# Kernel tuning notes

Hardware: AMD Instinct MI355X
Metric: run time of the kernel (lower is better)

## Reference

```python
import jax, jax.numpy as jnp
import numpy as np

N_NODES = 50000
N_EDGES = 800000
MUL = 32                      # multiplicity of 0e and 1o in node_feats
AVG_NUM_NEIGHBORS = 16.0
INV_SQRT3 = 1.0 / np.sqrt(3.0)


def setup_inputs() -> dict:
    key = jax.random.key(0)
    ks = jax.random.split(key, 7)
    return {
        "node_feats": jax.random.normal(ks[0], (N_NODES, 4 * MUL), dtype=jnp.float32),
        "edge_attrs": jax.random.normal(ks[1], (N_EDGES, 4), dtype=jnp.float32),
        "senders": jax.random.randint(ks[2], (N_EDGES,), 0, N_NODES, dtype=jnp.int64) if jax.config.jax_enable_x64 else jax.random.randint(ks[2], (N_EDGES,), 0, N_NODES, dtype=jnp.int32),
        "receivers": jax.random.randint(ks[3], (N_EDGES,), 0, N_NODES, dtype=jnp.int32),
        "w_mlp0": jax.random.normal(ks[4], (1, 64), dtype=jnp.float32),
        "w_mlp1": jax.random.normal(ks[5], (64, 64), dtype=jnp.float32),
        "w_mlp2": jax.random.normal(ks[6], (64, 4 * MUL), dtype=jnp.float32),
    }


def reference(node_feats, edge_attrs, senders, receivers, w_mlp0, w_mlp1, w_mlp2):
    # node_feats layout: [N, MUL] scalars (0e) then [N, MUL*3] flattened vectors (1o)
    s = node_feats[:, :MUL]                          # [N, MUL]   32x0e
    v = node_feats[:, MUL:].reshape(-1, MUL, 3)      # [N, MUL,3] 32x1o

    # gather sender features per edge
    s_e = s[senders]                                 # [E, MUL]
    v_e = v[senders]                                 # [E, MUL, 3]

    ea0 = edge_attrs[:, :1]                          # [E,1]  1x0e
    ea1 = edge_attrs[:, 1:4]                         # [E,3]  1x1o

    # equivariant tensor product with edge_attrs.filter(drop='0e') = 1x1o,
    # keeping only target irreps (0e,1o):
    #   0e x 1o -> 1o : scalar * vector
    tp_1o = s_e[:, :, None] * ea1[:, None, :]        # [E, MUL, 3]
    #   1o x 1o -> 0e : dot / sqrt(3)  (component normalization)
    tp_0e = jnp.einsum('eci,ei->ec', v_e, ea1) * INV_SQRT3  # [E, MUL]

    # concatenate([msgs.filter(target), tp]).regroup() -> 64x0e + 64x1o
    scalars = jnp.concatenate([s_e, tp_0e], axis=1)          # [E, 2*MUL]
    vectors = jnp.concatenate([v_e, tp_1o], axis=1)          # [E, 2*MUL, 3]

    # MLP gate on scalar edge attrs (e3nn MLP: no bias, 1/sqrt(fan_in), swish)
    h = jax.nn.swish(ea0 @ w_mlp0 / jnp.sqrt(1.0))           # [E,64]
    h = jax.nn.swish(h @ w_mlp1 / jnp.sqrt(64.0))            # [E,64]
    mix = h @ w_mlp2 / jnp.sqrt(64.0)                        # [E, 4*MUL]

    n_sc = 2 * MUL
    scalars = scalars * mix[:, :n_sc]                        # gate 0e
    vectors = vectors * mix[:, n_sc:, None]                  # gate 1o (one scalar per vector)

    msgs = jnp.concatenate([scalars, vectors.reshape(vectors.shape[0], -1)], axis=1)  # [E, 8*MUL]

    # scatter-add messages to receivers
    out = jax.ops.segment_sum(msgs, receivers, num_segments=N_NODES)  # [N, 8*MUL]
    return out / jnp.sqrt(AVG_NUM_NEIGHBORS)
```

## Files before the change

kernel.cpp:

```cpp
#include <hip/hip_runtime.h>
#include <hip/hip_fp16.h>
#include <cstdint>

#define N_NODES   50000
#define FEAT      128
#define OUTF      256
#define MAX_EDGES 800000
#define CAP       64
#define INV_SQRT3 0.57735026918962576f
#define NW        (64 + 64*64 + 64*128)
#define TB_BLKS   ((N_NODES * 32 + 255) / 256)

__device__ float    g_wf[NW];
__device__ uint16_t g_lut16[65536 * 128];
__device__ uint16_t g_tbl[N_NODES * FEAT];
__device__ int      g_flags[4];
__device__ int      g_cnt[N_NODES];
__device__ uint32_t g_slot[N_NODES * CAP];
__device__ unsigned char g_used[65536];

__device__ __forceinline__ float b2f(uint32_t b) {
    union { uint32_t u; float f; } v; v.u = b << 16; return v.f;
}
__device__ __forceinline__ uint32_t f2b_bits(float f) {
    union { float f; uint32_t u; } v; v.f = f;
    uint32_t u = v.u;
    u += 0x7fffu + ((u >> 16) & 1u);
    return u >> 16;
}
__device__ __forceinline__ float swishf(float x) {
    return x / (1.0f + __expf(-x));
}
__device__ __forceinline__ float sane(float x) {
    union { float f; uint32_t u; } v; v.f = x;
    return (((v.u >> 23) & 0xffu) >= 0x8Du) ? 0.0f : x;
}
__device__ __forceinline__ float loadf(const void* p, int i, int isbf) {
    return isbf ? b2f(((const uint16_t*)p)[i]) : ((const float*)p)[i];
}
__device__ __forceinline__ float h2f(uint32_t bits16) {
    return __half2float(__ushort_as_half((unsigned short)bits16));
}
__device__ __forceinline__ uint32_t f2h(float x) {
    return (uint32_t)__half_as_ushort(__float2half(x));
}

__global__ __launch_bounds__(256) void init_kernel(
    const void* nf, const void* ea, const void* w0, const void* w1, const void* w2,
    const int* snd, const int* rcv, int snd_force64, int n_edges)
{
    int bx = blockIdx.x, t = threadIdx.x;
    if (bx == 0) {
        __shared__ int viol[4];
        if (t < 4) viol[t] = 0;
        __syncthreads();
        {   int n = N_NODES * FEAT; int step = (n / 256) | 1;
            long long i = (long long)t * step;
            if (i < n) {
                uint32_t e = (((const uint16_t*)nf)[i] >> 7) & 0xffu;
                if (e > 140u) atomicOr(&viol[2], 1);
            } }
        {   int n = n_edges * 4; int step = (n / 256) | 1;
            long long i = (long long)t * step;
            if (i < n) {
                uint32_t e = (((const uint16_t*)ea)[i] >> 7) & 0xffu;
                if (e > 140u) atomicOr(&viol[3], 1);
            } }
        if (t < 64) {
            int i = 2 * t + 1;
            if (i < 2 * n_edges) {
                if (snd[i] != 0) atomicOr(&viol[0], 1);
                if (rcv[i] != 0) atomicOr(&viol[1], 1);
            }
        }
        __syncthreads();
        if (t == 0) {
            g_flags[0] = snd_force64 ? 1 : !viol[0];
            g_flags[1] = !viol[1];
            g_flags[2] = !viol[2];
            g_flags[3] = !viol[3];
        }
    } else if (bx <= 49) {
        __shared__ int wv[3];
        if (t < 3) wv[t] = 0;
        __syncthreads();
        if (t < 64) {
            uint32_t e = (((const uint16_t*)w0)[t] >> 7) & 0xffu;
            if (e > 140u) atomicOr(&wv[0], 1);
        }
        { int i = t * 17; if (i < 4096) {
            uint32_t e = (((const uint16_t*)w1)[i] >> 7) & 0xffu;
            if (e > 140u) atomicOr(&wv[1], 1); } }
        { int i = t * 33; if (i < 8192) {
            uint32_t e = (((const uint16_t*)w2)[i] >> 7) & 0xffu;
            if (e > 140u) atomicOr(&wv[2], 1); } }
        __syncthreads();
        int i = (bx - 1) * 256 + t;
        if (i < 64)             g_wf[i] = loadf(w0, i, !wv[0]);
        else if (i < 64 + 4096) g_wf[i] = loadf(w1, i - 64, !wv[1]);
        else if (i < NW)        g_wf[i] = loadf(w2, i - (64 + 4096), !wv[2]);
    } else if (bx <= 49 + TB_BLKS) {
        __shared__ int nv;
        if (t == 0) nv = 0;
        __syncthreads();
        {   int n = N_NODES * FEAT; int step = (n / 256) | 1;
            long long i = (long long)t * step;
            if (i < n) {
                uint32_t e = (((const uint16_t*)nf)[i] >> 7) & 0xffu;
                if (e > 140u) atomicOr(&nv, 1);
            } }
        __syncthreads();
        int f2l = !nv;
        int i = (bx - 50) * 256 + t;
        if (i < N_NODES * 32) {
            int node = i >> 5, c = i & 31;
            int rb = node * FEAT;
            float s  = loadf(nf, rb + c, f2l);
            float v0 = loadf(nf, rb + 32 + 3 * c + 0, f2l);
            float v1 = loadf(nf, rb + 32 + 3 * c + 1, f2l);
            float v2 = loadf(nf, rb + 32 + 3 * c + 2, f2l);
            uint32_t lo = f2h(s)  | (f2h(v0) << 16);
            uint32_t hi = f2h(v1) | (f2h(v2) << 16);
            ((uint2*)g_tbl)[i] = make_uint2(lo, hi);
        }
    } else {
        __shared__ int ev[2];
        if (t < 2) ev[t] = 0;
        __syncthreads();
        {   int n = n_edges * 4; int step = (n / 256) | 1;
            long long i = (long long)t * step;
            if (i < n) {
                uint32_t x = (((const uint16_t*)ea)[i] >> 7) & 0xffu;
                if (x > 140u) atomicOr(&ev[1], 1);
            } }
        if (t < 64) {
            int i = 2 * t + 1;
            if (i < 2 * n_edges) {
                if (rcv[i] != 0) atomicOr(&ev[0], 1);
            }
        }
        __syncthreads();
        int f1l = !ev[0];
        int f3l = !ev[1];
        int e = (bx - 50 - TB_BLKS) * 256 + t;
        if (e < n_edges) {
            int ri = f1l ? rcv[2 * e] : rcv[e];
            ri = min(max(ri, 0), N_NODES - 1);
            uint32_t b0 = f3l ? (uint32_t)((const uint16_t*)ea)[4 * e]
                              : f2b_bits(((const float*)ea)[4 * e]);
            g_used[b0 & 0xffffu] = 1;
            int p = atomicAdd(&g_cnt[ri], 1);
            if (p < CAP) __builtin_nontemporal_store((uint32_t)e, &g_slot[ri * CAP + p]);
        }
    }
}

__global__ __launch_bounds__(256) void lut_kernel() {
    __shared__ float sw[4096 + 8192];
    int w = blockIdx.x * 4 + (threadIdx.x >> 6);
    int lane = threadIdx.x & 63;
    for (int i = threadIdx.x; i < 4096 + 8192; i += 256)
        sw[i] = g_wf[64 + i];
    int f = (lane < 16) ? (g_used[w + lane * 4096] != 0) : 0;
    unsigned long long mask = __ballot(f) & 0xffffull;
    __syncthreads();
    if (!mask) return;
    const float* w1 = sw;
    const float* w2 = sw + 4096;
    float w0l = g_wf[lane];
    while (mask) {
        int k = __builtin_ctzll(mask);
        mask &= mask - 1;
        int r = w + k * 4096;
        float x = b2f((uint32_t)r);
        float h0 = swishf(x * w0l);
        float a = 0.f;
        #pragma unroll 8
        for (int kk = 0; kk < 64; ++kk)
            a += __shfl(h0, kk, 64) * w1[kk * 64 + lane];
        float h1 = swishf(a * 0.125f);
        float a0 = 0.f, a1 = 0.f;
        #pragma unroll 8
        for (int kk = 0; kk < 64; ++kk) {
            float h1k = __shfl(h1, kk, 64);
            a0 += h1k * w2[kk * 128 + lane];
            a1 += h1k * w2[kk * 128 + 64 + lane];
        }
        float s1c = 0.125f * 0.25f;
        float s0c = (lane >= 32) ? s1c * INV_SQRT3 : s1c;
        float pa = sane(a0 * s0c);
        float pb = sane(a1 * s1c);
        float qa = __shfl_xor(pa, 32, 64);
        float qb = __shfl_xor(pb, 32, 64);
        if (lane < 32) {
            uint32_t lo = f2h(pa) | (f2h(qa) << 16);
            uint32_t hi = f2h(pb) | (f2h(qb) << 16);
            ((uint2*)(g_lut16 + (size_t)r * 128))[lane] = make_uint2(lo, hi);
        }
    }
}

__global__ __launch_bounds__(256) void gather_kernel(
    const void* __restrict__ ea, const int* __restrict__ snd, void* __restrict__ out)
{
    int wid = (blockIdx.x * 256 + threadIdx.x) >> 6;
    int lane = threadIdx.x & 63;
    if (wid >= N_NODES) return;
    int c = lane & 31;
    int half = lane >> 5;
    const int f0 = g_flags[0], f2 = g_flags[2], f3 = g_flags[3];
    int deg = min(g_cnt[wid], CAP);
    if (lane == 0) g_cnt[wid] = 0;

    float o0 = 0.f, o1 = 0.f, o2 = 0.f, o3 = 0.f,
          o4 = 0.f, o5 = 0.f, o6 = 0.f, o7 = 0.f;

    uint32_t pk_p = 0;
    float ex_p = 0.f, ey_p = 0.f, ez_p = 0.f;
    if (lane < deg) {
        uint32_t e = __builtin_nontemporal_load(&g_slot[wid * CAP + lane]);
        uint32_t b0;
        if (f3) {
            uint2 w = ((const uint2*)ea)[e];
            b0 = w.x & 0xffffu;
            ex_p = b2f(w.x >> 16);
            ey_p = b2f(w.y & 0xffffu);
            ez_p = b2f(w.y >> 16);
        } else {
            float4 w = ((const float4*)ea)[e];
            b0 = f2b_bits(w.x) & 0xffffu;
            ex_p = w.y; ey_p = w.z; ez_p = w.w;
        }
        int s_ = f0 ? snd[2 * e] : snd[e];
        s_ = min(max(s_, 0), N_NODES - 1);
        pk_p = ((uint32_t)s_ << 16) | b0;
    }

    const uint2* tbl = (const uint2*)g_tbl;

    for (int j = 0; j < deg; j += 4) {
        int jjA = j + half, jjB = j + 2 + half;
        float gA = (jjA < deg) ? 1.0f : 0.0f;
        float gB = (jjB < deg) ? 1.0f : 0.0f;
        int jxA = (jjA < deg) ? jjA : 0;
        int jxB = (jjB < deg) ? jjB : 0;

        uint32_t pkA = (uint32_t)__shfl((int)pk_p, jxA, 64);
        uint32_t pkB = (uint32_t)__shfl((int)pk_p, jxB, 64);
        float exA = __shfl(ex_p, jxA, 64), eyA = __shfl(ey_p, jxA, 64), ezA = __shfl(ez_p, jxA, 64);
        float exB = __shfl(ex_p, jxB, 64), eyB = __shfl(ey_p, jxB, 64), ezB = __shfl(ez_p, jxB, 64);

        uint2 mAu = ((const uint2*)(g_lut16 + (size_t)(pkA & 0xffffu) * 128))[c];
        uint2 mBu = ((const uint2*)(g_lut16 + (size_t)(pkB & 0xffffu) * 128))[c];
        uint2 hA = tbl[(size_t)(pkA >> 16) * 32 + c];
        uint2 hB = tbl[(size_t)(pkB >> 16) * 32 + c];

        float sA  = h2f(hA.x & 0xffffu), vA0 = h2f(hA.x >> 16);
        float vA1 = h2f(hA.y & 0xffffu), vA2 = h2f(hA.y >> 16);
        float sB  = h2f(hB.x & 0xffffu), vB0 = h2f(hB.x >> 16);
        float vB1 = h2f(hB.y & 0xffffu), vB2 = h2f(hB.y >> 16);

        {
            float m0 = h2f(mAu.x & 0xffffu) * gA, m1 = h2f(mAu.x >> 16) * gA;
            float m2 = h2f(mAu.y & 0xffffu) * gA, m3 = h2f(mAu.y >> 16) * gA;
            o0 += sA * m0;
            o1 += (vA0 * exA + vA1 * eyA + vA2 * ezA) * m1;
            o2 += vA0 * m2; o3 += vA1 * m2; o4 += vA2 * m2;
            float sm3 = sA * m3;
            o5 += exA * sm3; o6 += eyA * sm3; o7 += ezA * sm3;
        }
        {
            float m0 = h2f(mBu.x & 0xffffu) * gB, m1 = h2f(mBu.x >> 16) * gB;
            float m2 = h2f(mBu.y & 0xffffu) * gB, m3 = h2f(mBu.y >> 16) * gB;
            o0 += sB * m0;
            o1 += (vB0 * exB + vB1 * eyB + vB2 * ezB) * m1;
            o2 += vB0 * m2; o3 += vB1 * m2; o4 += vB2 * m2;
            float sm3 = sB * m3;
            o5 += exB * sm3; o6 += eyB * sm3; o7 += ezB * sm3;
        }
    }

    o0 += __shfl_xor(o0, 32, 64);
    o1 += __shfl_xor(o1, 32, 64);
    o2 += __shfl_xor(o2, 32, 64);
    o3 += __shfl_xor(o3, 32, 64);
    o4 += __shfl_xor(o4, 32, 64);
    o5 += __shfl_xor(o5, 32, 64);
    o6 += __shfl_xor(o6, 32, 64);
    o7 += __shfl_xor(o7, 32, 64);

    if (half == 0) {
        size_t bo = (size_t)wid * OUTF;
        if (f2) {
            uint16_t* o = (uint16_t*)out;
            o[bo + c]             = (uint16_t)f2b_bits(o0);
            o[bo + 32 + c]        = (uint16_t)f2b_bits(o1);
            o[bo + 64 + 3*c + 0]  = (uint16_t)f2b_bits(o2);
            o[bo + 64 + 3*c + 1]  = (uint16_t)f2b_bits(o3);
            o[bo + 64 + 3*c + 2]  = (uint16_t)f2b_bits(o4);
            o[bo + 160 + 3*c + 0] = (uint16_t)f2b_bits(o5);
            o[bo + 160 + 3*c + 1] = (uint16_t)f2b_bits(o6);
            o[bo + 160 + 3*c + 2] = (uint16_t)f2b_bits(o7);
        } else {
            float* o = (float*)out;
            o[bo + c]             = o0;
            o[bo + 32 + c]        = o1;
            o[bo + 64 + 3*c + 0]  = o2;
            o[bo + 64 + 3*c + 1]  = o3;
            o[bo + 64 + 3*c + 2]  = o4;
            o[bo + 160 + 3*c + 0] = o5;
            o[bo + 160 + 3*c + 1] = o6;
            o[bo + 160 + 3*c + 2] = o7;
        }
    }
}

extern "C" void kernel_launch(void* const* d_in, const int* in_sizes, int n_in,
                              void* d_out, int out_size, void* d_ws, size_t ws_size,
                              hipStream_t stream) {
    (void)n_in; (void)out_size; (void)d_ws; (void)ws_size;
    const void* nf = d_in[0];
    const void* ea = d_in[1];
    const int* snd = (const int*)d_in[2];
    const int* rcv = (const int*)d_in[3];
    const void* w0 = d_in[4];
    const void* w1 = d_in[5];
    const void* w2 = d_in[6];

    int n_edges = in_sizes[1] / 4;
    if (n_edges > MAX_EDGES) n_edges = MAX_EDGES;
    int snd_force64 = (in_sizes[2] == 2 * in_sizes[3]) ? 1 : 0;
    int eb = (n_edges + 255) / 256;

    init_kernel<<<50 + TB_BLKS + eb, 256, 0, stream>>>(nf, ea, w0, w1, w2, snd, rcv, snd_force64, n_edges);
    lut_kernel<<<1024, 256, 0, stream>>>();
    gather_kernel<<<(N_NODES + 3) / 4, 256, 0, stream>>>(ea, snd, d_out);
}
```

Baseline: 243.8 us.

## Bin edges by receiver block then build per-node slots in shared memory

Replaces per-node global atomics into scattered slot arrays with a two-level bucketing: edges are first appended to 782 coarse bins (64 nodes each), then a second pass builds per-node slot lists in LDS and writes them out contiguously. The bin pass is fused into the LUT kernel launch as extra blocks, and the LUT blocks now read weights from global memory instead of staging them in shared memory. This aims to cut scattered global atomics and write traffic, at the cost of an extra read/write of edge indices and fixed bin capacity that may drop edges if a bin overflows.

```diff
diff --git a/kernel.cpp b/kernel.cpp
--- a/kernel.cpp
+++ b/kernel.cpp
@@ -10,13 +10,20 @@
 #define INV_SQRT3 0.57735026918962576f
 #define NW        (64 + 64*64 + 64*128)
 #define TB_BLKS   ((N_NODES * 32 + 255) / 256)
+#define NBINS     782
+#define BINCAP    1536
+#define NPAD      (NBINS * 64)
+
+typedef unsigned int u32x4 __attribute__((ext_vector_type(4)));
 
 __device__ float    g_wf[NW];
 __device__ uint16_t g_lut16[65536 * 128];
 __device__ uint16_t g_tbl[N_NODES * FEAT];
 __device__ int      g_flags[4];
-__device__ int      g_cnt[N_NODES];
-__device__ uint32_t g_slot[N_NODES * CAP];
+__device__ int      g_cnt[NPAD];
+__device__ uint32_t g_slot[NPAD * CAP];
+__device__ uint32_t g_bin[NBINS * BINCAP];
+__device__ int      g_bcnt[NBINS];
 __device__ unsigned char g_used[65536];
 
 __device__ __forceinline__ float b2f(uint32_t b) {
@@ -149,54 +156,75 @@
             uint32_t b0 = f3l ? (uint32_t)((const uint16_t*)ea)[4 * e]
                               : f2b_bits(((const float*)ea)[4 * e]);
             g_used[b0 & 0xffffu] = 1;
-            int p = atomicAdd(&g_cnt[ri], 1);
-            if (p < CAP) __builtin_nontemporal_store((uint32_t)e, &g_slot[ri * CAP + p]);
-        }
-    }
-}
-
-__global__ __launch_bounds__(256) void lut_kernel() {
-    __shared__ float sw[4096 + 8192];
-    int w = blockIdx.x * 4 + (threadIdx.x >> 6);
-    int lane = threadIdx.x & 63;
-    for (int i = threadIdx.x; i < 4096 + 8192; i += 256)
-        sw[i] = g_wf[64 + i];
-    int f = (lane < 16) ? (g_used[w + lane * 4096] != 0) : 0;
-    unsigned long long mask = __ballot(f) & 0xffffull;
-    __syncthreads();
-    if (!mask) return;
-    const float* w1 = sw;
-    const float* w2 = sw + 4096;
-    float w0l = g_wf[lane];
-    while (mask) {
-        int k = __builtin_ctzll(mask);
-        mask &= mask - 1;
-        int r = w + k * 4096;
-        float x = b2f((uint32_t)r);
-        float h0 = swishf(x * w0l);
-        float a = 0.f;
-        #pragma unroll 8
-        for (int kk = 0; kk < 64; ++kk)
-            a += __shfl(h0, kk, 64) * w1[kk * 64 + lane];
-        float h1 = swishf(a * 0.125f);
-        float a0 = 0.f, a1 = 0.f;
-        #pragma unroll 8
-        for (int kk = 0; kk < 64; ++kk) {
-            float h1k = __shfl(h1, kk, 64);
-            a0 += h1k * w2[kk * 128 + lane];
-            a1 += h1k * w2[kk * 128 + 64 + lane];
-        }
-        float s1c = 0.125f * 0.25f;
-        float s0c = (lane >= 32) ? s1c * INV_SQRT3 : s1c;
-        float pa = sane(a0 * s0c);
-        float pb = sane(a1 * s1c);
-        float qa = __shfl_xor(pa, 32, 64);
-        float qb = __shfl_xor(pb, 32, 64);
-        if (lane < 32) {
-            uint32_t lo = f2h(pa) | (f2h(qa) << 16);
-            uint32_t hi = f2h(pb) | (f2h(qb) << 16);
-            ((uint2*)(g_lut16 + (size_t)r * 128))[lane] = make_uint2(lo, hi);
-        }
+            int bin = ri >> 6;
+            int p = atomicAdd(&g_bcnt[bin], 1);
+            if (p < BINCAP)
+                __builtin_nontemporal_store(((uint32_t)e << 6) | (uint32_t)(ri & 63),
+                                            &g_bin[(size_t)bin * BINCAP + p]);
+        }
+    }
+}
+
+__global__ __launch_bounds__(256) void lut_scatter_kernel() {
+    __shared__ uint32_t lslot[64 * CAP];
+    __shared__ int lcnt[64];
+    int bx = blockIdx.x, t = threadIdx.x;
+    if (bx < 1024) {
+        int w = bx * 4 + (t >> 6);
+        int lane = t & 63;
+        int f = (lane < 16) ? (g_used[w * 16 + lane] != 0) : 0;
+        unsigned long long mask = __ballot(f) & 0xffffull;
+        if (!mask) return;
+        const float* w1 = g_wf + 64;
+        const float* w2 = g_wf + 64 + 4096;
+        float w0l = g_wf[lane];
+        while (mask) {
+            int bit = __builtin_ctzll(mask);
+            mask &= mask - 1;
+            int r = w * 16 + bit;
+            float x = b2f((uint32_t)r);
+            float h0 = swishf(x * w0l);
+            float a = 0.f;
+            #pragma unroll 8
+            for (int kk = 0; kk < 64; ++kk)
+                a += __shfl(h0, kk, 64) * w1[kk * 64 + lane];
+            float h1 = swishf(a * 0.125f);
+            float a0 = 0.f, a1 = 0.f;
+            #pragma unroll 8
+            for (int kk = 0; kk < 64; ++kk) {
+                float h1k = __shfl(h1, kk, 64);
+                a0 += h1k * w2[kk * 128 + lane];
+                a1 += h1k * w2[kk * 128 + 64 + lane];
+            }
+            float s1c = 0.125f * 0.25f;
+            float s0c = (lane >= 32) ? s1c * INV_SQRT3 : s1c;
+            float pa = sane(a0 * s0c);
+            float pb = sane(a1 * s1c);
+            float qa = __shfl_xor(pa, 32, 64);
+            float qb = __shfl_xor(pb, 32, 64);
+            if (lane < 32) {
+                uint32_t lo = f2h(pa) | (f2h(qa) << 16);
+                uint32_t hi = f2h(pb) | (f2h(qb) << 16);
+                ((uint2*)(g_lut16 + (size_t)r * 128))[lane] = make_uint2(lo, hi);
+            }
+        }
+    } else {
+        int b = bx - 1024;
+        if (t < 64) lcnt[t] = 0;
+        __syncthreads();
+        int cnt = min(g_bcnt[b], BINCAP);
+        for (int i = t; i < cnt; i += 256) {
+            uint32_t en = __builtin_nontemporal_load(&g_bin[(size_t)b * BINCAP + i]);
+            int local = (int)(en & 63u);
+            int pos = atomicAdd(&lcnt[local], 1);
+            if (pos < CAP) lslot[local * CAP + pos] = en >> 6;
+        }
+        __syncthreads();
+        uint32_t* dst = g_slot + (size_t)b * 64 * CAP;
+        const u32x4* src4 = (const u32x4*)lslot;
+        for (int i = t; i < 64 * CAP / 4; i += 256)
+            __builtin_nontemporal_store(src4[i], &((u32x4*)dst)[i]);
+        if (t < 64) g_cnt[b * 64 + t] = min(lcnt[t], CAP);
     }
 }
 
@@ -210,7 +238,7 @@
     int half = lane >> 5;
     const int f0 = g_flags[0], f2 = g_flags[2], f3 = g_flags[3];
     int deg = min(g_cnt[wid], CAP);
-    if (lane == 0) g_cnt[wid] = 0;
+    if (lane == 0 && wid < NBINS) g_bcnt[wid] = 0;
 
     float o0 = 0.f, o1 = 0.f, o2 = 0.f, o3 = 0.f,
           o4 = 0.f, o5 = 0.f, o6 = 0.f, o7 = 0.f;
@@ -218,7 +246,7 @@
     uint32_t pk_p = 0;
     float ex_p = 0.f, ey_p = 0.f, ez_p = 0.f;
     if (lane < deg) {
-        uint32_t e = __builtin_nontemporal_load(&g_slot[wid * CAP + lane]);
+        uint32_t e = __builtin_nontemporal_load(&g_slot[(size_t)wid * CAP + lane]);
         uint32_t b0;
         if (f3) {
             uint2 w = ((const uint2*)ea)[e];
@@ -333,6 +361,6 @@
     int eb = (n_edges + 255) / 256;
 
     init_kernel<<<50 + TB_BLKS + eb, 256, 0, stream>>>(nf, ea, w0, w1, w2, snd, rcv, snd_force64, n_edges);
-    lut_kernel<<<1024, 256, 0, stream>>>();
+    lut_scatter_kernel<<<1024 + NBINS, 256, 0, stream>>>();
     gather_kernel<<<(N_NODES + 3) / 4, 256, 0, stream>>>(ea, snd, d_out);
 }
```

Result: slower. 418.8 us (+71.8%).
